# Kernel optimization log

Measured on AMD Instinct MI355X. Metric: run time of the kernel, lower is better.

The kernel has to match this reference:

```python
import jax, jax.numpy as jnp
import numpy as np

L, B, H, D, S, FF = 24, 4, 16, 512, 4096, 2048
HD = D // H
POS = 2048  # current kv_cache_len (write position)
EPS = 1e-5
SCALE = 1.0 / np.sqrt(HD)


def layer_norm(x, w, b):
    m = jnp.mean(x, axis=-1, keepdims=True)
    v = jnp.mean(jnp.square(x - m), axis=-1, keepdims=True)
    return (x - m) * jax.lax.rsqrt(v + EPS) * w + b


def setup_inputs() -> dict:
    key = jax.random.key(0)
    ks = jax.random.split(key, 12)
    f = lambda k, shape: jax.random.normal(k, shape, dtype=jnp.float32) * 0.02
    # decode mask: positions [0, POS] are attendable (index_fill_ sets POS True)
    attn_mask = jnp.broadcast_to(jnp.arange(S) <= POS, (B, H, 1, S))
    return {
        "x": jax.random.normal(ks[0], (B, 1, D), dtype=jnp.float32),
        "k_cache": jax.random.normal(ks[1], (L, B, H, S, HD), dtype=jnp.float32),
        "v_cache": jax.random.normal(ks[2], (L, B, H, S, HD), dtype=jnp.float32),
        "attn_mask": attn_mask,
        "qkv_w": f(ks[3], (L, 3 * D, D)),
        "qkv_b": f(ks[4], (L, 3 * D)),
        "out_w": f(ks[5], (L, D, D)),
        "out_b": f(ks[6], (L, D)),
        "mlp_w1": f(ks[7], (L, FF, D)),
        "mlp_b1": f(ks[8], (L, FF)),
        "mlp_w2": f(ks[9], (L, D, FF)),
        "mlp_b2": f(ks[10], (L, D)),
        "norm_w1": jnp.ones((L, D), jnp.float32),
        "norm_b1": jnp.zeros((L, D), jnp.float32),
        "norm_w2": jnp.ones((L, D), jnp.float32),
        "norm_b2": jnp.zeros((L, D), jnp.float32),
        "kv_cache_len": POS,
    }


def reference(x, k_cache, v_cache, attn_mask, qkv_w, qkv_b, out_w, out_b,
              mlp_w1, mlp_b1, mlp_w2, mlp_b2, norm_w1, norm_b1, norm_w2,
              norm_b2, kv_cache_len):
    pos = kv_cache_len

    def block(h, p):
        kc0, vc0, qw, qb, ow, ob, w1, b1, w2, b2, nw1, nb1, nw2, nb2 = p
        qkv = h @ qw.T + qb                      # [B,1,3D]
        q, k, v = jnp.split(qkv, 3, axis=-1)
        q = q.reshape(B, 1, H, HD).transpose(0, 2, 1, 3)   # [B,H,1,HD]
        k = k.reshape(B, 1, H, HD).transpose(0, 2, 1, 3)
        v = v.reshape(B, 1, H, HD).transpose(0, 2, 1, 3)
        # in-place cache update at write position (index_copy_ on dim 2)
        kc = kc0.at[:, :, pos, :].set(k[:, :, 0, :])       # [B,H,S,HD]
        vc = vc0.at[:, :, pos, :].set(v[:, :, 0, :])
        scores = jnp.einsum('bhqd,bhkd->bhqk', q, kc) * SCALE
        scores = jnp.where(attn_mask, scores, -1e9)
        attn = jnp.einsum('bhqk,bhkd->bhqd', jax.nn.softmax(scores, axis=-1), vc)
        attn = attn.transpose(0, 2, 1, 3).reshape(B, 1, D)
        attn = attn @ ow.T + ob
        h = layer_norm(h + attn, nw1, nb1)
        mlp = jax.nn.relu(h @ w1.T + b1) @ w2.T + b2
        h = layer_norm(h + mlp, nw2, nb2)
        return h, None

    xs = (k_cache, v_cache, qkv_w, qkv_b, out_w, out_b, mlp_w1, mlp_b1,
          mlp_w2, mlp_b2, norm_w1, norm_b1, norm_w2, norm_b2)
    out, _ = jax.lax.scan(block, x, xs)
    return out
```

## Files before the change

### kernel.cpp

```cpp
#include <hip/hip_runtime.h>


#define DEV __device__ __forceinline__

static constexpr int LNUM = 24;
static constexpr int B = 4;
static constexpr int H = 16;
static constexpr int D = 512;
static constexpr int S = 4096;
static constexpr int FF = 2048;
static constexpr int HD = 32;
static constexpr int NCH = 9;
static constexpr int NBLK = 512;
static constexpr float EPS = 1e-5f;
static constexpr float SCALE = 0.17677669529663687f;

DEV float dot4(float4 a, float4 b) { return a.x*b.x + a.y*b.y + a.z*b.z + a.w*b.w; }

DEV float gld(const float* p) {
    return __hip_atomic_load((float*)p, __ATOMIC_RELAXED, __HIP_MEMORY_SCOPE_AGENT);
}
DEV void gst(float* p, float v) {
    __hip_atomic_store(p, v, __ATOMIC_RELAXED, __HIP_MEMORY_SCOPE_AGENT);
}
DEV void gadd(float* p, float v) {
    __hip_atomic_fetch_add(p, v, __ATOMIC_RELAXED, __HIP_MEMORY_SCOPE_AGENT);
}
DEV float2 gld2(const float* p) {
    unsigned long long v = __hip_atomic_load((const unsigned long long*)p,
                                             __ATOMIC_RELAXED, __HIP_MEMORY_SCOPE_AGENT);
    float2 r;
    r.x = __uint_as_float((unsigned)v);
    r.y = __uint_as_float((unsigned)(v >> 32));
    return r;
}

DEV float waveReduceSum(float v) {
#pragma unroll
    for (int o = 32; o > 0; o >>= 1) v += __shfl_xor(v, o);
    return v;
}
DEV float waveReduceMax(float v) {
#pragma unroll
    for (int o = 32; o > 0; o >>= 1) v = fmaxf(v, __shfl_xor(v, o));
    return v;
}
DEV float blockReduceSum(float v, volatile float* red) {
    v = waveReduceSum(v);
    __syncthreads();
    if ((threadIdx.x & 63) == 0) red[threadIdx.x >> 6] = v;
    __syncthreads();
    return red[0] + red[1] + red[2] + red[3];
}
DEV float blockReduceMax(float v, volatile float* red) {
    v = waveReduceMax(v);
    __syncthreads();
    if ((threadIdx.x & 63) == 0) red[threadIdx.x >> 6] = v;
    __syncthreads();
    return fmaxf(fmaxf(red[0], red[1]), fmaxf(red[2], red[3]));
}

DEV void g_arrive(unsigned* ctr) {
    __syncthreads();
    if (threadIdx.x == 0)
        __hip_atomic_fetch_add(ctr, 1u, __ATOMIC_RELAXED, __HIP_MEMORY_SCOPE_AGENT);
}
DEV void g_wait(unsigned* ctr, unsigned target) {
    if (threadIdx.x == 0) {
        while (__hip_atomic_load(ctr, __ATOMIC_RELAXED, __HIP_MEMORY_SCOPE_AGENT) < target)
            __builtin_amdgcn_s_sleep(1);
    }
    __syncthreads();
}

struct Params {
    const float *x, *kc, *vc;
    const float *qkvw, *qkvb, *outw, *outb, *w1, *b1, *w2, *b2;
    const float *nw1, *nb1, *nw2, *nb2;
    const int* posp;
    float *num, *den, *t1, *m1, *sbuf, *out;
    float *stats;
    unsigned* bar;
};

__global__ __launch_bounds__(256, 2) void mega(Params p) {
    const int blk = blockIdx.x;
    const int b = blk >> 7;
    const int gblk = blk & 127;
    const int tid = threadIdx.x;
    const int w = tid >> 6;
    const int lane = tid & 63;
    const int pos = p.posp[0];

    __shared__ float SM[2308];
    float* red = SM + 2304;

    float* numG  = p.num + (size_t)b * LNUM * 512;
    float* denG  = p.den + (size_t)b * LNUM * 16;
    float* t1g   = p.t1 + (b << 9);
    float* m1g   = p.m1 + (b << 11);
    float* sbufg = p.sbuf + (b << 9);
    unsigned* ctr = p.bar + (size_t)b * 64;
    float* stT1 = p.stats + b * 96;
    float* stSB = p.stats + b * 96 + 48;
    unsigned nb_ = 0;

    const int h = gblk >> 3, c = gblk & 7;
    const int bh = (b << 4) + h;

    for (int l = 0; l < LNUM; ++l) {
        const float* hsrc = (l == 0) ? (p.x + (b << 9)) : sbufg;
        const bool aln = (l > 0);
        const float* pnw = p.nw2 + (aln ? (size_t)(l - 1) * 512 : 0);
        const float* pnb = p.nb2 + (aln ? (size_t)(l - 1) * 512 : 0);
        const float* qwL = p.qkvw + (size_t)l * 1536 * 512;
        const float* qbL = p.qkvb + (size_t)l * 1536;
        const float* kcL = p.kc + (size_t)l * 8388608;
        const float* vcL = p.vc + (size_t)l * 8388608;
        const float* owL = p.outw + (size_t)l * 512 * 512;
        const float* obL = p.outb + (size_t)l * 512;
        const float* w1L = p.w1 + (size_t)l * 2048 * 512;
        const float* b1L = p.b1 + (size_t)l * 2048;
        const float* w2L = p.w2 + (size_t)l * 512 * 2048;
        const float* b2L = p.b2 + (size_t)l * 512;
        const float* n1w = p.nw1 + (size_t)l * 512;
        const float* n1b = p.nb1 + (size_t)l * 512;
        float* numL = numG + (size_t)l * 512;
        float* denL = denG + (size_t)l * 16;

        {
            const int pp2 = (c << 8) + tid;
            float4 kpre[8];
            {
                const float4* kp = (const float4*)(kcL + ((size_t)bh * 4096 + pp2) * 32);
#pragma unroll
                for (int i = 0; i < 8; ++i) kpre[i] = kp[i];
            }
            float vpre[32];
            {
                const float* vp = vcL + ((size_t)bh * 4096 + (c << 8) + ((tid >> 5) << 5)) * 32 + (tid & 31);
#pragma unroll
                for (int i = 0; i < 32; ++i) vpre[i] = vp[(size_t)i * 32];
            }
            if (l) g_wait(ctr, nb_ * 128);

            {
                float2 hv = gld2(hsrc + 2 * tid);
                if (aln) {
                    float ss = gld(stSB + (l - 1) * 2), sq = gld(stSB + (l - 1) * 2 + 1);
                    float mean = ss * (1.f / 512.f);
                    float rs = rsqrtf(sq * (1.f / 512.f) - mean * mean + EPS);
                    float2 gw = ((const float2*)pnw)[tid];
                    float2 gb = ((const float2*)pnb)[tid];
                    SM[2 * tid]     = (hv.x - mean) * rs * gw.x + gb.x;
                    SM[2 * tid + 1] = (hv.y - mean) * rs * gw.y + gb.y;
                } else {
                    SM[2 * tid] = hv.x;
                    SM[2 * tid + 1] = hv.y;
                }
            }
            __syncthreads();

            const int qd = tid >> 3, s8 = tid & 7;
            {
                const float4* wr = (const float4*)(qwL + (size_t)((h << 5) + qd) * 512) + s8 * 16;
                const float4* hh4 = (const float4*)SM + s8 * 16;
                float a = 0.f;
#pragma unroll
                for (int i = 0; i < 16; ++i) a += dot4(wr[i], hh4[i]);
                a += __shfl_xor(a, 1); a += __shfl_xor(a, 2); a += __shfl_xor(a, 4);
                if (s8 == 0) SM[1032 + qd] = (a + qbL[(h << 5) + qd]) * SCALE;
            }
            if (c == 7) {
                {
                    const float4* wr = (const float4*)(qwL + (size_t)(512 + (h << 5) + qd) * 512) + s8 * 16;
                    const float4* hh4 = (const float4*)SM + s8 * 16;
                    float a = 0.f;
#pragma unroll
                    for (int i = 0; i < 16; ++i) a += dot4(wr[i], hh4[i]);
                    a += __shfl_xor(a, 1); a += __shfl_xor(a, 2); a += __shfl_xor(a, 4);
                    if (s8 == 0) SM[1064 + qd] = a + qbL[512 + (h << 5) + qd];
                }
                {
                    const float4* wr = (const float4*)(qwL + (size_t)(1024 + (h << 5) + qd) * 512) + s8 * 16;
                    const float4* hh4 = (const float4*)SM + s8 * 16;
                    float a = 0.f;
#pragma unroll
                    for (int i = 0; i < 16; ++i) a += dot4(wr[i], hh4[i]);
                    a += __shfl_xor(a, 1); a += __shfl_xor(a, 2); a += __shfl_xor(a, 4);
                    if (s8 == 0) SM[1096 + qd] = a + qbL[1024 + (h << 5) + qd];
                }
            }
            __syncthreads();

            float* qs = SM + 1032;
            float sc = 0.f;
#pragma unroll
            for (int i = 0; i < 8; ++i)
                sc += qs[4 * i] * kpre[i].x + qs[4 * i + 1] * kpre[i].y
                    + qs[4 * i + 2] * kpre[i].z + qs[4 * i + 3] * kpre[i].w;
            const bool act = pp2 < pos;
            float e = act ? expf(sc) : 0.f;
            if (tid == 0) {
                float en = 0.f;
                if (c == 7) {
                    float snew = 0.f;
                    for (int j = 0; j < 32; ++j) snew += qs[j] * SM[1064 + j];
                    en = expf(snew);
                }
                SM[1128] = en;
            }
            SM[512 + tid] = e;
            float den = blockReduceSum(e, red) + SM[1128];

            const int d = tid & 31, g = tid >> 5;
            float acc = 0.f;
#pragma unroll
            for (int i = 0; i < 32; ++i) acc += SM[512 + (g << 5) + i] * vpre[i];
            if (c == 7 && g == 0) acc += SM[1128] * SM[1096 + d];
            SM[768 + g * 33 + d] = acc;
            __syncthreads();
            if (tid < 32) {
                float o = 0.f;
#pragma unroll
                for (int gg = 0; gg < 8; ++gg) o += SM[768 + gg * 33 + tid];
                gadd(numL + (h << 5) + tid, o);
                if (tid == 0) gadd(denL + h, den);
            }
            g_arrive(ctr); ++nb_;
        }

        {
            const int dd = (gblk << 2) + w;
            float4 oA, oB;
            {
                const float4* wr4 = (const float4*)(owL + (size_t)dd * 512);
                oA = wr4[lane]; oB = wr4[lane + 64];
            }
            float mean = 0.f, rs = 1.f;
            if (aln) {
                float ss = gld(stSB + (l - 1) * 2), sq = gld(stSB + (l - 1) * 2 + 1);
                mean = ss * (1.f / 512.f);
                rs = rsqrtf(sq * (1.f / 512.f) - mean * mean + EPS);
            }
            g_wait(ctr, nb_ * 128);

            {
                float2 nv = gld2(numL + 2 * tid);
                SM[2 * tid] = nv.x; SM[2 * tid + 1] = nv.y;
                if (tid < 8) {
                    float2 dv = gld2(denL + 2 * tid);
                    SM[512 + 2 * tid] = dv.x; SM[512 + 2 * tid + 1] = dv.y;
                }
            }
            __syncthreads();
            {
                float inv = 1.f / SM[512 + (tid >> 4)];
                SM[2 * tid] *= inv; SM[2 * tid + 1] *= inv;
            }
            __syncthreads();
            const float4* as4 = (const float4*)SM;
            float acc = dot4(oA, as4[lane]) + dot4(oB, as4[lane + 64]);
            acc = waveReduceSum(acc);
            if (lane == 0) {
                float hv = gld(hsrc + dd);
                if (aln) hv = (hv - mean) * rs * pnw[dd] + pnb[dd];
                float tv = hv + acc + obL[dd];
                gst(t1g + dd, tv);
                SM[1024 + w] = tv;
            }
            __syncthreads();
            if (tid == 0) {
                float s = SM[1024] + SM[1025] + SM[1026] + SM[1027];
                float q = SM[1024] * SM[1024] + SM[1025] * SM[1025]
                        + SM[1026] * SM[1026] + SM[1027] * SM[1027];
                gadd(stT1 + l * 2, s);
                gadd(stT1 + l * 2 + 1, q);
            }
            g_arrive(ctr); ++nb_;
        }

        {
            const int rr = (gblk << 4) + (tid >> 4);
            const int s16 = tid & 15;
            float4 w1pre[8];
            {
                const float4* wr = (const float4*)(w1L + (size_t)rr * 512) + s16 * 8;
#pragma unroll
                for (int i = 0; i < 8; ++i) w1pre[i] = wr[i];
            }
            float bv = b1L[rr];
            g_wait(ctr, nb_ * 128);

            {
                float2 tv2 = gld2(t1g + 2 * tid);
                float ss = gld(stT1 + l * 2), sq = gld(stT1 + l * 2 + 1);
                float mean = ss * (1.f / 512.f);
                float rs = rsqrtf(sq * (1.f / 512.f) - mean * mean + EPS);
                float2 gw = ((const float2*)n1w)[tid];
                float2 gb = ((const float2*)n1b)[tid];
                SM[2 * tid]     = (tv2.x - mean) * rs * gw.x + gb.x;
                SM[2 * tid + 1] = (tv2.y - mean) * rs * gw.y + gb.y;
            }
            __syncthreads();
            const float4* hh4 = (const float4*)SM + s16 * 8;
            float a = 0.f;
#pragma unroll
            for (int i = 0; i < 8; ++i) a += dot4(w1pre[i], hh4[i]);
            a += __shfl_xor(a, 1); a += __shfl_xor(a, 2);
            a += __shfl_xor(a, 4); a += __shfl_xor(a, 8);
            if (s16 == 0) gst(m1g + rr, fmaxf(a + bv, 0.f));
            g_arrive(ctr); ++nb_;
        }

        {
            const int dd = (gblk << 2) + w;
            float4 w2pre[8];
            {
                const float4* wr4 = (const float4*)(w2L + (size_t)dd * 2048);
#pragma unroll
                for (int i = 0; i < 8; ++i) w2pre[i] = wr4[(i << 6) + lane];
            }
            float tv = 0.f, gw = 0.f, gb = 0.f, bv = 0.f;
            if (lane == 0) { tv = gld(t1g + dd); gw = n1w[dd]; gb = n1b[dd]; bv = b2L[dd]; }
            float ss = gld(stT1 + l * 2), sq = gld(stT1 + l * 2 + 1);
            float mean = ss * (1.f / 512.f);
            float rs = rsqrtf(sq * (1.f / 512.f) - mean * mean + EPS);
            g_wait(ctr, nb_ * 128);

#pragma unroll
            for (int j = 0; j < 4; ++j) {
                float2 mv = gld2(m1g + 8 * tid + 2 * j);
                SM[8 * tid + 2 * j] = mv.x;
                SM[8 * tid + 2 * j + 1] = mv.y;
            }
            __syncthreads();
            const float4* ms4 = (const float4*)SM;
            float acc = 0.f;
#pragma unroll
            for (int i = 0; i < 8; ++i) acc += dot4(w2pre[i], ms4[(i << 6) + lane]);
            acc = waveReduceSum(acc);
            if (lane == 0) {
                float hl = (tv - mean) * rs * gw + gb;
                float sv = hl + acc + bv;
                gst(sbufg + dd, sv);
                SM[2048 + w] = sv;
            }
            __syncthreads();
            if (tid == 0) {
                float s = SM[2048] + SM[2049] + SM[2050] + SM[2051];
                float q = SM[2048] * SM[2048] + SM[2049] * SM[2049]
                        + SM[2050] * SM[2050] + SM[2051] * SM[2051];
                gadd(stSB + l * 2, s);
                gadd(stSB + l * 2 + 1, q);
            }
            g_arrive(ctr); ++nb_;
        }
    }

    if (gblk == 0) {
        g_wait(ctr, nb_ * 128);
        const float* nw = p.nw2 + 23 * 512;
        const float* nbv = p.nb2 + 23 * 512;
        float a0 = gld(sbufg + tid), a1 = gld(sbufg + tid + 256);
        float ss = gld(stSB + 23 * 2), sq = gld(stSB + 23 * 2 + 1);
        float mean = ss * (1.f / 512.f);
        float rs = rsqrtf(sq * (1.f / 512.f) - mean * mean + EPS);
        p.out[(b << 9) + tid] = (a0 - mean) * rs * nw[tid] + nbv[tid];
        p.out[(b << 9) + 256 + tid] = (a1 - mean) * rs * nw[tid + 256] + nbv[tid + 256];
    }
}

__global__ __launch_bounds__(256) void k_qkv(
    const float* __restrict__ hsrc, int apply_ln,
    const float* __restrict__ nw, const float* __restrict__ nb,
    const float* __restrict__ w, const float* __restrict__ bias,
    float* __restrict__ qkv)
{
    const int lane = threadIdx.x & 63;
    const int wid = (blockIdx.x << 2) + (threadIdx.x >> 6);
    const int b = wid / 1536;
    const int r = wid - b * 1536;
    const float* hb = hsrc + (b << 9);
    const int k0 = lane << 3;
    float4 h0 = *(const float4*)(hb + k0);
    float4 h1 = *(const float4*)(hb + k0 + 4);
    float hv[8] = {h0.x, h0.y, h0.z, h0.w, h1.x, h1.y, h1.z, h1.w};
    if (apply_ln) {
        float s = 0.f, s2 = 0.f;
#pragma unroll
        for (int j = 0; j < 8; ++j) { s += hv[j]; s2 += hv[j] * hv[j]; }
        s = waveReduceSum(s);
        s2 = waveReduceSum(s2);
        float mean = s * (1.f / 512.f);
        float rs = rsqrtf(s2 * (1.f / 512.f) - mean * mean + EPS);
        float4 nw0 = *(const float4*)(nw + k0);
        float4 nw1 = *(const float4*)(nw + k0 + 4);
        float4 nb0 = *(const float4*)(nb + k0);
        float4 nb1 = *(const float4*)(nb + k0 + 4);
        float nwv[8] = {nw0.x, nw0.y, nw0.z, nw0.w, nw1.x, nw1.y, nw1.z, nw1.w};
        float nbv[8] = {nb0.x, nb0.y, nb0.z, nb0.w, nb1.x, nb1.y, nb1.z, nb1.w};
#pragma unroll
        for (int j = 0; j < 8; ++j) hv[j] = (hv[j] - mean) * rs * nwv[j] + nbv[j];
    }
    const float* wr = w + (size_t)r * 512 + k0;
    float4 w0 = *(const float4*)(wr);
    float4 w1 = *(const float4*)(wr + 4);
    float acc = w0.x * hv[0] + w0.y * hv[1] + w0.z * hv[2] + w0.w * hv[3]
              + w1.x * hv[4] + w1.y * hv[5] + w1.z * hv[6] + w1.w * hv[7];
    acc = waveReduceSum(acc);
    if (lane == 0) {
        float v = acc + bias[r];
        if (r < 512) v *= SCALE;
        qkv[b * 1536 + r] = v;
    }
}

__global__ __launch_bounds__(256) void k_attn(
    const float* __restrict__ kc, const float* __restrict__ vc,
    const float* __restrict__ qkv, float* __restrict__ part,
    const int* __restrict__ posp)
{
    const int tid = threadIdx.x;
    const int c = blockIdx.x % NCH;
    const int bh = blockIdx.x / NCH;
    const int b = bh >> 4, h = bh & 15;
    const int pos = posp[0];
    __shared__ float qs[32];
    __shared__ float es[256];
    __shared__ float red[4];
    __shared__ float op[8][33];
    if (tid < 32) qs[tid] = qkv[b * 1536 + h * 32 + tid];
    __syncthreads();
    float score = -1e30f;
    bool act = false;
    if (c < 8) {
        int p = c * 256 + tid;
        act = (p < pos);
        const float4* kp = (const float4*)(kc + ((size_t)bh * S + p) * HD);
        float s = 0.f;
#pragma unroll
        for (int i = 0; i < 8; ++i) {
            float4 kv = kp[i];
            s += qs[4 * i] * kv.x + qs[4 * i + 1] * kv.y + qs[4 * i + 2] * kv.z + qs[4 * i + 3] * kv.w;
        }
        if (act) score = s;
    } else if (tid == 0) {
        act = true;
        const float* kp = qkv + b * 1536 + 512 + h * 32;
        float s = 0.f;
#pragma unroll
        for (int j = 0; j < 32; ++j) s += qs[j] * kp[j];
        score = s;
    }
    float m = blockReduceMax(score, red);
    float e = act ? expf(score - m) : 0.f;
    es[tid] = e;
    float l = blockReduceSum(e, red);
    const int d = tid & 31, g = tid >> 5;
    float acc = 0.f;
    if (c < 8) {
        const float* vp = vc + ((size_t)bh * S + c * 256 + g * 32) * HD + d;
#pragma unroll 8
        for (int i = 0; i < 32; ++i) acc += es[g * 32 + i] * vp[(size_t)i * HD];
    } else if (g == 0) {
        acc = es[0] * qkv[b * 1536 + 1024 + h * 32 + d];
    }
    op[g][d] = acc;
    __syncthreads();
    if (tid < 32) {
        float o = 0.f;
#pragma unroll
        for (int gg = 0; gg < 8; ++gg) o += op[gg][tid];
        float* pp = part + (size_t)(bh * NCH + c) * 34;
        pp[2 + tid] = o;
        if (tid == 0) { pp[0] = m; pp[1] = l; }
    }
}

__global__ __launch_bounds__(256) void k_outproj(
    const float* __restrict__ part,
    const float* __restrict__ ow, const float* __restrict__ ob,
    const float* __restrict__ hsrc, int apply_ln,
    const float* __restrict__ nw, const float* __restrict__ nb,
    float* __restrict__ t1)
{
    const int tid = threadIdx.x;
    const int b = blockIdx.x >> 5;
    const int oc = blockIdx.x & 31;
    __shared__ float attn_s[512];
    __shared__ float hln[512];
    __shared__ float mh[16], sh[16];
    __shared__ float red[4];
    if (tid < 16) {
        const float* pp = part + (size_t)(b * 16 + tid) * NCH * 34;
        float m = -1e30f;
        for (int c = 0; c < NCH; ++c) m = fmaxf(m, pp[c * 34]);
        float ss = 0.f;
        for (int c = 0; c < NCH; ++c) ss += pp[c * 34 + 1] * expf(pp[c * 34] - m);
        mh[tid] = m;
        sh[tid] = ss;
    }
    __syncthreads();
#pragma unroll
    for (int e = tid; e < 512; e += 256) {
        int h = e >> 5, d = e & 31;
        const float* pp = part + (size_t)(b * 16 + h) * NCH * 34;
        float o = 0.f;
        for (int c = 0; c < NCH; ++c) o += pp[c * 34 + 2 + d] * expf(pp[c * 34] - mh[h]);
        attn_s[e] = o / sh[h];
    }
    float a0 = hsrc[(b << 9) + tid], a1 = hsrc[(b << 9) + 256 + tid];
    if (apply_ln) {
        float s = blockReduceSum(a0 + a1, red);
        float s2 = blockReduceSum(a0 * a0 + a1 * a1, red);
        float mean = s * (1.f / 512.f);
        float rs = rsqrtf(s2 * (1.f / 512.f) - mean * mean + EPS);
        hln[tid] = (a0 - mean) * rs * nw[tid] + nb[tid];
        hln[tid + 256] = (a1 - mean) * rs * nw[tid + 256] + nb[tid + 256];
    } else {
        hln[tid] = a0;
        hln[tid + 256] = a1;
    }
    __syncthreads();
    const int w = tid >> 6, lane = tid & 63, k0 = lane << 3;
#pragma unroll
    for (int oi = 0; oi < 4; ++oi) {
        int dd = (oc << 4) + (w << 2) + oi;
        const float4* wp = (const float4*)(ow + (size_t)dd * 512 + k0);
        float4 w0 = wp[0], w1 = wp[1];
        float acc = w0.x * attn_s[k0] + w0.y * attn_s[k0 + 1] + w0.z * attn_s[k0 + 2] + w0.w * attn_s[k0 + 3]
                  + w1.x * attn_s[k0 + 4] + w1.y * attn_s[k0 + 5] + w1.z * attn_s[k0 + 6] + w1.w * attn_s[k0 + 7];
        acc = waveReduceSum(acc);
        if (lane == 0) t1[(b << 9) + dd] = hln[dd] + acc + ob[dd];
    }
}

__global__ __launch_bounds__(256) void k_mlp1(
    const float* __restrict__ t1,
    const float* __restrict__ nw, const float* __restrict__ nb,
    const float* __restrict__ w1, const float* __restrict__ b1,
    float* __restrict__ m1)
{
    const int tid = threadIdx.x;
    const int b = blockIdx.x >> 7;
    const int oc = blockIdx.x & 127;
    __shared__ float hln[512];
    __shared__ float red[4];
    float a0 = t1[(b << 9) + tid], a1 = t1[(b << 9) + 256 + tid];
    float s = blockReduceSum(a0 + a1, red);
    float s2 = blockReduceSum(a0 * a0 + a1 * a1, red);
    float mean = s * (1.f / 512.f);
    float rs = rsqrtf(s2 * (1.f / 512.f) - mean * mean + EPS);
    hln[tid] = (a0 - mean) * rs * nw[tid] + nb[tid];
    hln[tid + 256] = (a1 - mean) * rs * nw[tid + 256] + nb[tid + 256];
    __syncthreads();
    const int w = tid >> 6, lane = tid & 63, k0 = lane << 3;
#pragma unroll
    for (int oi = 0; oi < 4; ++oi) {
        int r = (oc << 4) + (w << 2) + oi;
        const float4* wp = (const float4*)(w1 + (size_t)r * 512 + k0);
        float4 w0 = wp[0], w1v = wp[1];
        float acc = w0.x * hln[k0] + w0.y * hln[k0 + 1] + w0.z * hln[k0 + 2] + w0.w * hln[k0 + 3]
                  + w1v.x * hln[k0 + 4] + w1v.y * hln[k0 + 5] + w1v.z * hln[k0 + 6] + w1v.w * hln[k0 + 7];
        acc = waveReduceSum(acc);
        if (lane == 0) m1[(b << 11) + r] = fmaxf(acc + b1[r], 0.f);
    }
}

__global__ __launch_bounds__(256) void k_mlp2(
    const float* __restrict__ m1, const float* __restrict__ t1,
    const float* __restrict__ nw, const float* __restrict__ nb,
    const float* __restrict__ w2, const float* __restrict__ b2,
    float* __restrict__ sout)
{
    const int tid = threadIdx.x;
    const int b = blockIdx.x >> 7;
    const int oc = blockIdx.x & 127;
    __shared__ float ms[2048];
    __shared__ float red[4];
#pragma unroll
    for (int i = 0; i < 8; ++i) ms[tid + (i << 8)] = m1[(b << 11) + tid + (i << 8)];
    float a0 = t1[(b << 9) + tid], a1 = t1[(b << 9) + 256 + tid];
    float s = blockReduceSum(a0 + a1, red);
    float s2 = blockReduceSum(a0 * a0 + a1 * a1, red);
    float mean = s * (1.f / 512.f);
    float rs = rsqrtf(s2 * (1.f / 512.f) - mean * mean + EPS);
    const int w = tid >> 6, lane = tid & 63;
    const int dd = (oc << 2) + w;
    const float4* wp = (const float4*)(w2 + (size_t)dd * 2048);
    float acc = 0.f;
#pragma unroll
    for (int i = 0; i < 8; ++i) {
        int idx = (i << 6) + lane;
        float4 q = wp[idx];
        int k = idx << 2;
        acc += q.x * ms[k] + q.y * ms[k + 1] + q.z * ms[k + 2] + q.w * ms[k + 3];
    }
    acc = waveReduceSum(acc);
    if (lane == 0) {
        float td = t1[(b << 9) + dd];
        float hd = (td - mean) * rs * nw[dd] + nb[dd];
        sout[(b << 9) + dd] = hd + acc + b2[dd];
    }
}

__global__ __launch_bounds__(256) void k_finalln(
    const float* __restrict__ sbuf,
    const float* __restrict__ nw, const float* __restrict__ nb,
    float* __restrict__ out)
{
    const int b = blockIdx.x, tid = threadIdx.x;
    __shared__ float red[4];
    float a0 = sbuf[(b << 9) + tid], a1 = sbuf[(b << 9) + 256 + tid];
    float s = blockReduceSum(a0 + a1, red);
    float s2 = blockReduceSum(a0 * a0 + a1 * a1, red);
    float mean = s * (1.f / 512.f);
    float rs = rsqrtf(s2 * (1.f / 512.f) - mean * mean + EPS);
    out[(b << 9) + tid] = (a0 - mean) * rs * nw[tid] + nb[tid];
    out[(b << 9) + 256 + tid] = (a1 - mean) * rs * nw[tid + 256] + nb[tid + 256];
}

extern "C" void kernel_launch(void* const* d_in, const int* in_sizes, int n_in,
                              void* d_out, int out_size, void* d_ws, size_t ws_size,
                              hipStream_t stream)
{
    const float* x    = (const float*)d_in[0];
    const float* kc   = (const float*)d_in[1];
    const float* vc   = (const float*)d_in[2];
    const float* qkvw = (const float*)d_in[4];
    const float* qkvb = (const float*)d_in[5];
    const float* outw = (const float*)d_in[6];
    const float* outb = (const float*)d_in[7];
    const float* w1   = (const float*)d_in[8];
    const float* b1   = (const float*)d_in[9];
    const float* w2   = (const float*)d_in[10];
    const float* b2   = (const float*)d_in[11];
    const float* nw1  = (const float*)d_in[12];
    const float* nb1  = (const float*)d_in[13];
    const float* nw2  = (const float*)d_in[14];
    const float* nb2  = (const float*)d_in[15];
    const int*   posp = (const int*)d_in[16];

    int dev = 0, cu = 0, nb = 0;
    hipGetDevice(&dev);
    hipDeviceGetAttribute(&cu, hipDeviceAttributeMultiprocessorCount, dev);
    hipOccupancyMaxActiveBlocksPerMultiprocessor(&nb, (const void*)mega, 256, 0);
    const bool coop_ok = ((long)nb * cu >= NBLK);

    float* ws = (float*)d_ws;

    if (coop_ok) {
        Params prm;
        prm.x = x; prm.kc = kc; prm.vc = vc;
        prm.qkvw = qkvw; prm.qkvb = qkvb; prm.outw = outw; prm.outb = outb;
        prm.w1 = w1; prm.b1 = b1; prm.w2 = w2; prm.b2 = b2;
        prm.nw1 = nw1; prm.nb1 = nb1; prm.nw2 = nw2; prm.nb2 = nb2;
        prm.posp = posp;
        prm.bar   = (unsigned*)ws;
        prm.stats = ws + 256;
        prm.num   = ws + 640;
        prm.den   = ws + 49792;
        prm.t1    = ws + 51328;
        prm.m1    = ws + 53376;
        prm.sbuf  = ws + 61568;
        prm.out   = (float*)d_out;
        hipMemsetAsync(ws, 0, 63616 * sizeof(float), stream);
        void* args[] = { &prm };
        hipLaunchCooperativeKernel(reinterpret_cast<const void*>(&mega),
                                   dim3(NBLK), dim3(256), args, 0, stream);
        return;
    }

    float* qkvbuf = ws;
    float* part   = qkvbuf + 6144;
    float* t1     = part + 19584;
    float* m1     = t1 + 2048;
    float* sbuf   = m1 + 8192;
    const size_t kvLayerStride = (size_t)B * H * S * HD;

    for (int l = 0; l < LNUM; ++l) {
        const float* hsrc = (l == 0) ? x : sbuf;
        const int aln = (l > 0) ? 1 : 0;
        const float* pnw = (l > 0) ? (nw2 + (size_t)(l - 1) * 512) : nullptr;
        const float* pnb = (l > 0) ? (nb2 + (size_t)(l - 1) * 512) : nullptr;

        k_qkv<<<1536, 256, 0, stream>>>(hsrc, aln, pnw, pnb,
                                        qkvw + (size_t)l * 1536 * 512,
                                        qkvb + (size_t)l * 1536, qkvbuf);
        k_attn<<<B * H * NCH, 256, 0, stream>>>(kc + (size_t)l * kvLayerStride,
                                                vc + (size_t)l * kvLayerStride,
                                                qkvbuf, part, posp);
        k_outproj<<<B * 32, 256, 0, stream>>>(part,
                                              outw + (size_t)l * 512 * 512,
                                              outb + (size_t)l * 512,
                                              hsrc, aln, pnw, pnb, t1);
        k_mlp1<<<B * 128, 256, 0, stream>>>(t1,
                                            nw1 + (size_t)l * 512, nb1 + (size_t)l * 512,
                                            w1 + (size_t)l * FF * D, b1 + (size_t)l * FF, m1);
        k_mlp2<<<B * 128, 256, 0, stream>>>(m1, t1,
                                            nw1 + (size_t)l * 512, nb1 + (size_t)l * 512,
                                            w2 + (size_t)l * D * FF, b2 + (size_t)l * 512, sbuf);
    }
    k_finalln<<<B, 256, 0, stream>>>(sbuf, nw2 + 23 * 512, nb2 + 23 * 512, (float*)d_out);
}
```

Measured before the change: 843.2 us.

## Fuse MLP down-projection into up-projection phase with atomic partials, drop a grid barrier

```diff
diff --git a/kernel.cpp b/kernel.cpp
--- a/kernel.cpp
+++ b/kernel.cpp
@@ -20,10 +20,16 @@
 DEV float gld(const float* p) {
     return __hip_atomic_load((float*)p, __ATOMIC_RELAXED, __HIP_MEMORY_SCOPE_AGENT);
 }
+DEV unsigned gldu(const unsigned* p) {
+    return __hip_atomic_load((unsigned*)p, __ATOMIC_RELAXED, __HIP_MEMORY_SCOPE_AGENT);
+}
 DEV void gst(float* p, float v) {
     __hip_atomic_store(p, v, __ATOMIC_RELAXED, __HIP_MEMORY_SCOPE_AGENT);
 }
 DEV void gadd(float* p, float v) {
+    __hip_atomic_fetch_add(p, v, __ATOMIC_RELAXED, __HIP_MEMORY_SCOPE_AGENT);
+}
+DEV void gaddu(unsigned* p, unsigned v) {
     __hip_atomic_fetch_add(p, v, __ATOMIC_RELAXED, __HIP_MEMORY_SCOPE_AGENT);
 }
 DEV float2 gld2(const float* p) {
@@ -60,15 +66,9 @@
     return fmaxf(fmaxf(red[0], red[1]), fmaxf(red[2], red[3]));
 }
 
-DEV void g_arrive(unsigned* ctr) {
-    __syncthreads();
-    if (threadIdx.x == 0)
-        __hip_atomic_fetch_add(ctr, 1u, __ATOMIC_RELAXED, __HIP_MEMORY_SCOPE_AGENT);
-}
-DEV void g_wait(unsigned* ctr, unsigned target) {
+DEV void wait_cnt(unsigned* c, unsigned tgt) {
     if (threadIdx.x == 0) {
-        while (__hip_atomic_load(ctr, __ATOMIC_RELAXED, __HIP_MEMORY_SCOPE_AGENT) < target)
-            __builtin_amdgcn_s_sleep(1);
+        while (gldu(c) < tgt) __builtin_amdgcn_s_sleep(1);
     }
     __syncthreads();
 }
@@ -78,9 +78,9 @@
     const float *qkvw, *qkvb, *outw, *outb, *w1, *b1, *w2, *b2;
     const float *nw1, *nb1, *nw2, *nb2;
     const int* posp;
-    float *num, *den, *t1, *m1, *sbuf, *out;
-    float *stats;
-    unsigned* bar;
+    float* fbase;
+    unsigned* cnt;
+    float* out;
 };
 
 __global__ __launch_bounds__(256, 2) void mega(Params p) {
@@ -92,27 +92,22 @@
     const int lane = tid & 63;
     const int pos = p.posp[0];
 
-    __shared__ float SM[2308];
-    float* red = SM + 2304;
-
-    float* numG  = p.num + (size_t)b * LNUM * 512;
-    float* denG  = p.den + (size_t)b * LNUM * 16;
-    float* t1g   = p.t1 + (b << 9);
-    float* m1g   = p.m1 + (b << 11);
-    float* sbufg = p.sbuf + (b << 9);
-    unsigned* ctr = p.bar + (size_t)b * 64;
-    float* stT1 = p.stats + b * 96;
-    float* stSB = p.stats + b * 96 + 48;
-    unsigned nb_ = 0;
+    __shared__ float SM[1160];
+    float* red = SM + 1132;
+
+    float* G      = p.fbase + (size_t)b * 37728;
+    float* numden = G;
+    float* t1raw  = G + 13056;
+    float* t1st   = G + 25344;
+    float* sbst   = G + 25392;
+    float* mlpo   = G + 25440;
+    unsigned* cntG = p.cnt + (size_t)b * 288;
 
     const int h = gblk >> 3, c = gblk & 7;
     const int bh = (b << 4) + h;
+    const int s8 = tid & 7, qd = tid >> 3;
 
     for (int l = 0; l < LNUM; ++l) {
-        const float* hsrc = (l == 0) ? (p.x + (b << 9)) : sbufg;
-        const bool aln = (l > 0);
-        const float* pnw = p.nw2 + (aln ? (size_t)(l - 1) * 512 : 0);
-        const float* pnb = p.nb2 + (aln ? (size_t)(l - 1) * 512 : 0);
         const float* qwL = p.qkvw + (size_t)l * 1536 * 512;
         const float* qbL = p.qkvb + (size_t)l * 1536;
         const float* kcL = p.kc + (size_t)l * 8388608;
@@ -122,11 +117,12 @@
         const float* w1L = p.w1 + (size_t)l * 2048 * 512;
         const float* b1L = p.b1 + (size_t)l * 2048;
         const float* w2L = p.w2 + (size_t)l * 512 * 2048;
-        const float* b2L = p.b2 + (size_t)l * 512;
         const float* n1w = p.nw1 + (size_t)l * 512;
         const float* n1b = p.nb1 + (size_t)l * 512;
-        float* numL = numG + (size_t)l * 512;
-        float* denL = denG + (size_t)l * 16;
+        unsigned* cntA = cntG + l * 12;
+        unsigned* cntB = cntA + 4;
+        unsigned* cntC = cntA + 8;
+        float* ndL = numden + (size_t)l * 544;
 
         {
             const int pp2 = (c << 8) + tid;
@@ -142,32 +138,50 @@
 #pragma unroll
                 for (int i = 0; i < 32; ++i) vpre[i] = vp[(size_t)i * 32];
             }
-            if (l) g_wait(ctr, nb_ * 128);
-
-            {
-                float2 hv = gld2(hsrc + 2 * tid);
-                if (aln) {
-                    float ss = gld(stSB + (l - 1) * 2), sq = gld(stSB + (l - 1) * 2 + 1);
-                    float mean = ss * (1.f / 512.f);
-                    float rs = rsqrtf(sq * (1.f / 512.f) - mean * mean + EPS);
-                    float2 gw = ((const float2*)pnw)[tid];
-                    float2 gb = ((const float2*)pnb)[tid];
-                    SM[2 * tid]     = (hv.x - mean) * rs * gw.x + gb.x;
-                    SM[2 * tid + 1] = (hv.y - mean) * rs * gw.y + gb.y;
-                } else {
-                    SM[2 * tid] = hv.x;
-                    SM[2 * tid + 1] = hv.y;
+
+            if (l == 0) {
+                const float2* xb = (const float2*)(p.x + (b << 9));
+                float2 hv = xb[tid];
+                SM[2 * tid] = hv.x;
+                SM[2 * tid + 1] = hv.y;
+                __syncthreads();
+            } else {
+                wait_cnt(cntG + (l - 1) * 12 + 8, 128);
+                if (tid == 0) {
+                    float2 st = gld2(t1st + (l - 1) * 2);
+                    SM[1156] = st.x; SM[1157] = st.y;
                 }
-            }
-            __syncthreads();
-
-            const int qd = tid >> 3, s8 = tid & 7;
+                __syncthreads();
+                float mean1 = SM[1156] * (1.f / 512.f);
+                float rs1 = rsqrtf(SM[1157] * (1.f / 512.f) - mean1 * mean1 + EPS);
+                float2 tv = gld2(t1raw + (size_t)(l - 1) * 512 + 2 * tid);
+                float2 mo = gld2(mlpo + (size_t)(l - 1) * 512 + 2 * tid);
+                const float* n1wP = p.nw1 + (size_t)(l - 1) * 512;
+                const float* n1bP = p.nb1 + (size_t)(l - 1) * 512;
+                const float* b2P  = p.b2 + (size_t)(l - 1) * 512;
+                float sb0 = (tv.x - mean1) * rs1 * n1wP[2 * tid] + n1bP[2 * tid] + mo.x + b2P[2 * tid];
+                float sb1 = (tv.y - mean1) * rs1 * n1wP[2 * tid + 1] + n1bP[2 * tid + 1] + mo.y + b2P[2 * tid + 1];
+                float s = blockReduceSum(sb0 + sb1, red);
+                float q = blockReduceSum(sb0 * sb0 + sb1 * sb1, red);
+                if (gblk == 0 && tid == 0) {
+                    gst(sbst + (l - 1) * 2, s);
+                    gst(sbst + (l - 1) * 2 + 1, q);
+                }
+                float mean2 = s * (1.f / 512.f);
+                float rs2 = rsqrtf(q * (1.f / 512.f) - mean2 * mean2 + EPS);
+                const float* w2n = p.nw2 + (size_t)(l - 1) * 512;
+                const float* b2n = p.nb2 + (size_t)(l - 1) * 512;
+                SM[2 * tid]     = (sb0 - mean2) * rs2 * w2n[2 * tid] + b2n[2 * tid];
+                SM[2 * tid + 1] = (sb1 - mean2) * rs2 * w2n[2 * tid + 1] + b2n[2 * tid + 1];
+                __syncthreads();
+            }
+
             {
                 const float4* wr = (const float4*)(qwL + (size_t)((h << 5) + qd) * 512) + s8 * 16;
                 const float4* hh4 = (const float4*)SM + s8 * 16;
                 float a = 0.f;
 #pragma unroll
-                for (int i = 0; i < 16; ++i) a += dot4(wr[i], hh4[i]);
+                for (int j = 0; j < 16; ++j) { int i = (j + 2 * s8) & 15; a += dot4(wr[i], hh4[i]); }
                 a += __shfl_xor(a, 1); a += __shfl_xor(a, 2); a += __shfl_xor(a, 4);
                 if (s8 == 0) SM[1032 + qd] = (a + qbL[(h << 5) + qd]) * SCALE;
             }
@@ -177,7 +191,7 @@
                     const float4* hh4 = (const float4*)SM + s8 * 16;
                     float a = 0.f;
 #pragma unroll
-                    for (int i = 0; i < 16; ++i) a += dot4(wr[i], hh4[i]);
+                    for (int j = 0; j < 16; ++j) { int i = (j + 2 * s8) & 15; a += dot4(wr[i], hh4[i]); }
                     a += __shfl_xor(a, 1); a += __shfl_xor(a, 2); a += __shfl_xor(a, 4);
                     if (s8 == 0) SM[1064 + qd] = a + qbL[512 + (h << 5) + qd];
                 }
@@ -186,7 +200,7 @@
                     const float4* hh4 = (const float4*)SM + s8 * 16;
                     float a = 0.f;
 #pragma unroll
-                    for (int i = 0; i < 16; ++i) a += dot4(wr[i], hh4[i]);
+                    for (int j = 0; j < 16; ++j) { int i = (j + 2 * s8) & 15; a += dot4(wr[i], hh4[i]); }
                     a += __shfl_xor(a, 1); a += __shfl_xor(a, 2); a += __shfl_xor(a, 4);
                     if (s8 == 0) SM[1096 + qd] = a + qbL[1024 + (h << 5) + qd];
                 }
@@ -224,10 +238,11 @@
                 float o = 0.f;
 #pragma unroll
                 for (int gg = 0; gg < 8; ++gg) o += SM[768 + gg * 33 + tid];
-                gadd(numL + (h << 5) + tid, o);
-                if (tid == 0) gadd(denL + h, den);
-            }
-            g_arrive(ctr); ++nb_;
+                gadd(ndL + h * 34 + tid, o);
+                if (tid == 0) gadd(ndL + h * 34 + 32, den);
+            }
+            __syncthreads();
+            if (tid == 0) gaddu(cntA, 1u);
         }
 
         {
@@ -237,47 +252,57 @@
                 const float4* wr4 = (const float4*)(owL + (size_t)dd * 512);
                 oA = wr4[lane]; oB = wr4[lane + 64];
             }
-            float mean = 0.f, rs = 1.f;
-            if (aln) {
-                float ss = gld(stSB + (l - 1) * 2), sq = gld(stSB + (l - 1) * 2 + 1);
-                mean = ss * (1.f / 512.f);
-                rs = rsqrtf(sq * (1.f / 512.f) - mean * mean + EPS);
-            }
-            g_wait(ctr, nb_ * 128);
-
-            {
-                float2 nv = gld2(numL + 2 * tid);
-                SM[2 * tid] = nv.x; SM[2 * tid + 1] = nv.y;
-                if (tid < 8) {
-                    float2 dv = gld2(denL + 2 * tid);
-                    SM[512 + 2 * tid] = dv.x; SM[512 + 2 * tid + 1] = dv.y;
+            wait_cnt(cntA, 128);
+
+            float hv = 0.f;
+            if (lane == 0) {
+                if (l == 0) {
+                    hv = p.x[(b << 9) + dd];
+                } else {
+                    float2 st1 = gld2(t1st + (l - 1) * 2);
+                    float m1_ = st1.x * (1.f / 512.f);
+                    float r1_ = rsqrtf(st1.y * (1.f / 512.f) - m1_ * m1_ + EPS);
+                    float2 st2 = gld2(sbst + (l - 1) * 2);
+                    float m2_ = st2.x * (1.f / 512.f);
+                    float r2_ = rsqrtf(st2.y * (1.f / 512.f) - m2_ * m2_ + EPS);
+                    float tvp = gld(t1raw + (size_t)(l - 1) * 512 + dd);
+                    float mop = gld(mlpo + (size_t)(l - 1) * 512 + dd);
+                    const float* n1wP = p.nw1 + (size_t)(l - 1) * 512;
+                    const float* n1bP = p.nb1 + (size_t)(l - 1) * 512;
+                    const float* b2P  = p.b2 + (size_t)(l - 1) * 512;
+                    const float* w2n  = p.nw2 + (size_t)(l - 1) * 512;
+                    const float* b2n  = p.nb2 + (size_t)(l - 1) * 512;
+                    float raw = (tvp - m1_) * r1_ * n1wP[dd] + n1bP[dd] + mop + b2P[dd];
+                    hv = (raw - m2_) * r2_ * w2n[dd] + b2n[dd];
                 }
             }
-            __syncthreads();
-            {
-                float inv = 1.f / SM[512 + (tid >> 4)];
-                SM[2 * tid] *= inv; SM[2 * tid + 1] *= inv;
+            if (tid < 16) SM[512 + tid] = 1.f / gld(ndL + tid * 34 + 32);
+            __syncthreads();
+#pragma unroll
+            for (int k = 0; k < 2; ++k) {
+                int e = tid + (k << 8);
+                int h2 = e >> 5, d2 = e & 31;
+                SM[e] = gld(ndL + h2 * 34 + d2) * SM[512 + h2];
             }
             __syncthreads();
             const float4* as4 = (const float4*)SM;
             float acc = dot4(oA, as4[lane]) + dot4(oB, as4[lane + 64]);
             acc = waveReduceSum(acc);
             if (lane == 0) {
-                float hv = gld(hsrc + dd);
-                if (aln) hv = (hv - mean) * rs * pnw[dd] + pnb[dd];
-                float tv = hv + acc + obL[dd];
-                gst(t1g + dd, tv);
-                SM[1024 + w] = tv;
+                float tvv = hv + acc + obL[dd];
+                gst(t1raw + (size_t)l * 512 + dd, tvv);
+                SM[1152 + w] = tvv;
             }
             __syncthreads();
             if (tid == 0) {
-                float s = SM[1024] + SM[1025] + SM[1026] + SM[1027];
-                float q = SM[1024] * SM[1024] + SM[1025] * SM[1025]
-                        + SM[1026] * SM[1026] + SM[1027] * SM[1027];
-                gadd(stT1 + l * 2, s);
-                gadd(stT1 + l * 2 + 1, q);
-            }
-            g_arrive(ctr); ++nb_;
+                float s4 = SM[1152] + SM[1153] + SM[1154] + SM[1155];
+                float q4 = SM[1152] * SM[1152] + SM[1153] * SM[1153]
+                         + SM[1154] * SM[1154] + SM[1155] * SM[1155];
+                gadd(t1st + l * 2, s4);
+                gadd(t1st + l * 2 + 1, q4);
+            }
+            __syncthreads();
+            if (tid == 0) gaddu(cntB, 1u);
         }
 
         {
@@ -290,84 +315,73 @@
                 for (int i = 0; i < 8; ++i) w1pre[i] = wr[i];
             }
             float bv = b1L[rr];
-            g_wait(ctr, nb_ * 128);
-
+            wait_cnt(cntB, 128);
+
+            if (tid == 0) {
+                float2 st = gld2(t1st + l * 2);
+                SM[1156] = st.x; SM[1157] = st.y;
+            }
+            __syncthreads();
+            float mean = SM[1156] * (1.f / 512.f);
+            float rs = rsqrtf(SM[1157] * (1.f / 512.f) - mean * mean + EPS);
             {
-                float2 tv2 = gld2(t1g + 2 * tid);
-                float ss = gld(stT1 + l * 2), sq = gld(stT1 + l * 2 + 1);
-                float mean = ss * (1.f / 512.f);
-                float rs = rsqrtf(sq * (1.f / 512.f) - mean * mean + EPS);
+                float2 tv = gld2(t1raw + (size_t)l * 512 + 2 * tid);
                 float2 gw = ((const float2*)n1w)[tid];
                 float2 gb = ((const float2*)n1b)[tid];
-                SM[2 * tid]     = (tv2.x - mean) * rs * gw.x + gb.x;
-                SM[2 * tid + 1] = (tv2.y - mean) * rs * gw.y + gb.y;
+                SM[2 * tid]     = (tv.x - mean) * rs * gw.x + gb.x;
+                SM[2 * tid + 1] = (tv.y - mean) * rs * gw.y + gb.y;
             }
             __syncthreads();
             const float4* hh4 = (const float4*)SM + s16 * 8;
             float a = 0.f;
 #pragma unroll
-            for (int i = 0; i < 8; ++i) a += dot4(w1pre[i], hh4[i]);
+            for (int j = 0; j < 8; ++j) { int i = (j + s16) & 7; a += dot4(w1pre[i], hh4[i]); }
             a += __shfl_xor(a, 1); a += __shfl_xor(a, 2);
             a += __shfl_xor(a, 4); a += __shfl_xor(a, 8);
-            if (s16 == 0) gst(m1g + rr, fmaxf(a + bv, 0.f));
-            g_arrive(ctr); ++nb_;
+            if (s16 == 0) SM[1136 + (tid >> 4)] = fmaxf(a + bv, 0.f);
+            __syncthreads();
+#pragma unroll
+            for (int rep = 0; rep < 2; ++rep) {
+                int d = tid + (rep << 8);
+                const float4* wp = (const float4*)(w2L + (size_t)d * 2048 + (gblk << 4));
+                float pacc = 0.f;
+#pragma unroll
+                for (int j = 0; j < 4; ++j) {
+                    float4 q = wp[j];
+                    pacc += q.x * SM[1136 + 4 * j]     + q.y * SM[1136 + 4 * j + 1]
+                          + q.z * SM[1136 + 4 * j + 2] + q.w * SM[1136 + 4 * j + 3];
+                }
+                gadd(mlpo + (size_t)l * 512 + d, pacc);
+            }
+            __syncthreads();
+            if (tid == 0) gaddu(cntC, 1u);
         }
-
-        {
-            const int dd = (gblk << 2) + w;
-            float4 w2pre[8];
-            {
-                const float4* wr4 = (const float4*)(w2L + (size_t)dd * 2048);
-#pragma unroll
-                for (int i = 0; i < 8; ++i) w2pre[i] = wr4[(i << 6) + lane];
-            }
-            float tv = 0.f, gw = 0.f, gb = 0.f, bv = 0.f;
-            if (lane == 0) { tv = gld(t1g + dd); gw = n1w[dd]; gb = n1b[dd]; bv = b2L[dd]; }
-            float ss = gld(stT1 + l * 2), sq = gld(stT1 + l * 2 + 1);
-            float mean = ss * (1.f / 512.f);
-            float rs = rsqrtf(sq * (1.f / 512.f) - mean * mean + EPS);
-            g_wait(ctr, nb_ * 128);
-
-#pragma unroll
-            for (int j = 0; j < 4; ++j) {
-                float2 mv = gld2(m1g + 8 * tid + 2 * j);
-                SM[8 * tid + 2 * j] = mv.x;
-                SM[8 * tid + 2 * j + 1] = mv.y;
-            }
-            __syncthreads();
-            const float4* ms4 = (const float4*)SM;
-            float acc = 0.f;
-#pragma unroll
-            for (int i = 0; i < 8; ++i) acc += dot4(w2pre[i], ms4[(i << 6) + lane]);
-            acc = waveReduceSum(acc);
-            if (lane == 0) {
-                float hl = (tv - mean) * rs * gw + gb;
-                float sv = hl + acc + bv;
-                gst(sbufg + dd, sv);
-                SM[2048 + w] = sv;
-            }
-            __syncthreads();
-            if (tid == 0) {
-                float s = SM[2048] + SM[2049] + SM[2050] + SM[2051];
-                float q = SM[2048] * SM[2048] + SM[2049] * SM[2049]
-                        + SM[2050] * SM[2050] + SM[2051] * SM[2051];
-                gadd(stSB + l * 2, s);
-                gadd(stSB + l * 2 + 1, q);
-            }
-            g_arrive(ctr); ++nb_;
+    }
+
+    if (gblk == 0) {
+        wait_cnt(cntG + 23 * 12 + 8, 128);
+        if (tid == 0) {
+            float2 st = gld2(t1st + 23 * 2);
+            SM[1156] = st.x; SM[1157] = st.y;
         }
-    }
-
-    if (gblk == 0) {
-        g_wait(ctr, nb_ * 128);
-        const float* nw = p.nw2 + 23 * 512;
-        const float* nbv = p.nb2 + 23 * 512;
-        float a0 = gld(sbufg + tid), a1 = gld(sbufg + tid + 256);
-        float ss = gld(stSB + 23 * 2), sq = gld(stSB + 23 * 2 + 1);
-        float mean = ss * (1.f / 512.f);
-        float rs = rsqrtf(sq * (1.f / 512.f) - mean * mean + EPS);
-        p.out[(b << 9) + tid] = (a0 - mean) * rs * nw[tid] + nbv[tid];
-        p.out[(b << 9) + 256 + tid] = (a1 - mean) * rs * nw[tid + 256] + nbv[tid + 256];
+        __syncthreads();
+        float mean1 = SM[1156] * (1.f / 512.f);
+        float rs1 = rsqrtf(SM[1157] * (1.f / 512.f) - mean1 * mean1 + EPS);
+        float2 tv = gld2(t1raw + (size_t)23 * 512 + 2 * tid);
+        float2 mo = gld2(mlpo + (size_t)23 * 512 + 2 * tid);
+        const float* n1wP = p.nw1 + (size_t)23 * 512;
+        const float* n1bP = p.nb1 + (size_t)23 * 512;
+        const float* b2P  = p.b2 + (size_t)23 * 512;
+        float sb0 = (tv.x - mean1) * rs1 * n1wP[2 * tid] + n1bP[2 * tid] + mo.x + b2P[2 * tid];
+        float sb1 = (tv.y - mean1) * rs1 * n1wP[2 * tid + 1] + n1bP[2 * tid + 1] + mo.y + b2P[2 * tid + 1];
+        float s = blockReduceSum(sb0 + sb1, red);
+        float q = blockReduceSum(sb0 * sb0 + sb1 * sb1, red);
+        float mean2 = s * (1.f / 512.f);
+        float rs2 = rsqrtf(q * (1.f / 512.f) - mean2 * mean2 + EPS);
+        const float* w2n = p.nw2 + (size_t)23 * 512;
+        const float* b2n = p.nb2 + (size_t)23 * 512;
+        p.out[(b << 9) + 2 * tid]     = (sb0 - mean2) * rs2 * w2n[2 * tid] + b2n[2 * tid];
+        p.out[(b << 9) + 2 * tid + 1] = (sb1 - mean2) * rs2 * w2n[2 * tid + 1] + b2n[2 * tid + 1];
     }
 }
 
@@ -435,9 +449,9 @@
     float score = -1e30f;
     bool act = false;
     if (c < 8) {
-        int p = c * 256 + tid;
-        act = (p < pos);
-        const float4* kp = (const float4*)(kc + ((size_t)bh * S + p) * HD);
+        int pp = c * 256 + tid;
+        act = (pp < pos);
+        const float4* kp = (const float4*)(kc + ((size_t)bh * S + pp) * HD);
         float s = 0.f;
 #pragma unroll
         for (int i = 0; i < 8; ++i) {
@@ -456,7 +470,7 @@
     float m = blockReduceMax(score, red);
     float e = act ? expf(score - m) : 0.f;
     es[tid] = e;
-    float l = blockReduceSum(e, red);
+    float lsum = blockReduceSum(e, red);
     const int d = tid & 31, g = tid >> 5;
     float acc = 0.f;
     if (c < 8) {
@@ -474,7 +488,7 @@
         for (int gg = 0; gg < 8; ++gg) o += op[gg][tid];
         float* pp = part + (size_t)(bh * NCH + c) * 34;
         pp[2 + tid] = o;
-        if (tid == 0) { pp[0] = m; pp[1] = l; }
+        if (tid == 0) { pp[0] = m; pp[1] = lsum; }
     }
 }
 
@@ -657,15 +671,11 @@
         prm.w1 = w1; prm.b1 = b1; prm.w2 = w2; prm.b2 = b2;
         prm.nw1 = nw1; prm.nb1 = nb1; prm.nw2 = nw2; prm.nb2 = nb2;
         prm.posp = posp;
-        prm.bar   = (unsigned*)ws;
-        prm.stats = ws + 256;
-        prm.num   = ws + 640;
-        prm.den   = ws + 49792;
-        prm.t1    = ws + 51328;
-        prm.m1    = ws + 53376;
-        prm.sbuf  = ws + 61568;
+        prm.cnt   = (unsigned*)ws;
+        prm.fbase = ws + 1152;
         prm.out   = (float*)d_out;
-        hipMemsetAsync(ws, 0, 63616 * sizeof(float), stream);
+        const size_t initBytes = (1152 + 4 * 37728) * sizeof(float);
+        hipMemsetAsync(ws, 0, initBytes, stream);
         void* args[] = { &prm };
         hipLaunchCooperativeKernel(reinterpret_cast<const void*>(&mega),
                                    dim3(NBLK), dim3(256), args, 0, stream);
```

New measurement: 846.3 us. About the same (+0.4%).
